# Kernel tuning notes

Hardware: AMD Instinct MI355X
Metric: run time of the kernel (lower is better)

The kernel has to match this reference:

```python
import jax, jax.numpy as jnp
import numpy as np
import math

FEAT_DIM, M, K = 512, 64, 256
D = FEAT_DIM // M  # 8
ALPHA = 1.0
B = 16384


def setup_inputs() -> dict:
    key = jax.random.key(0)
    kx, kc = jax.random.split(key)
    x = jax.random.normal(kx, (B, FEAT_DIM), dtype=jnp.float32)
    # Codebook: unit-norm codewords scaled by 1/sqrt(M), mimicking the
    # normalized-hypersphere init (orthogonal rotation / permutation do not
    # change the math, only the values).
    c = jax.random.normal(kc, (M, K, D), dtype=jnp.float32)
    c = c / jnp.linalg.norm(c, axis=-1, keepdims=True) / math.sqrt(M)
    return {"x": x, "C": c}


def reference(x, C):
    # x: (B, feat_dim) -> (B, M, D)
    x_ = x.reshape(x.shape[0], M, D)
    # per-subspace inner products with codewords: (B, M, K)
    ips = jnp.einsum('bmd,mkd->bmk', x_, C)
    # training-mode straight-through assignment
    soft = jax.nn.softmax(ips * (M / ALPHA), axis=-1)
    hard = jax.nn.one_hot(jnp.argmax(ips, axis=-1), K, dtype=ips.dtype)
    codes = jax.lax.stop_gradient(hard - soft) + soft
    # reconstruction: (B, M, D) -> (B, feat_dim)
    x_hat = jnp.einsum('mkd,bmk->bmd', C, codes).reshape(x.shape[0], -1)
    return x_hat, codes
```

## Files before the change

### kernel.cpp

```cpp
#include <hip/hip_runtime.h>
#include <math.h>


#define B_SZ   16384
#define FEAT   512
#define M_SZ   64
#define K_SZ   256
#define D_SZ   8

typedef float v4f __attribute__((ext_vector_type(4)));

__global__ __launch_bounds__(256) void pq_argmax(
    const float* __restrict__ x,
    const float* __restrict__ C,
    unsigned char* __restrict__ bestk8)
{
#pragma clang fp contract(off)

    const int m     = blockIdx.x & (M_SZ - 1);
    const int chunk = blockIdx.x >> 6;
    const int b     = (chunk << 8) | threadIdx.x;

    const float* xp = x + (size_t)b * FEAT + m * D_SZ;
    const v4f xa = ((const v4f*)xp)[0];
    const v4f xb = ((const v4f*)xp)[1];

    const float* __restrict__ Cm = C + (size_t)m * (K_SZ * D_SZ);

    float best  = -INFINITY;
    int   bestk = 0;

#pragma unroll 8
    for (int k = 0; k < K_SZ; ++k) {
        const v4f* cr = (const v4f*)(Cm + k * D_SZ);
        const v4f ca = cr[0];
        const v4f cb = cr[1];
        v4f P = xa * ca;
        v4f Q = xb * cb;
        v4f T = P + Q;
        float dot = (T.x + T.y) + (T.z + T.w);
        if (dot > best) { best = dot; bestk = k; }
    }

    bestk8[(size_t)b * M_SZ + m] = (unsigned char)bestk;
}

__global__ __launch_bounds__(256) void pq_fill(
    const float* __restrict__ C,
    const unsigned char* __restrict__ bestk8,
    float* __restrict__ xhat,
    float* __restrict__ codes)
{
    const int t    = threadIdx.x;
    const int b0   = blockIdx.x << 2;
    const int w    = t >> 6;
    const int lane = t & 63;

    __shared__ unsigned char lbk[4 * M_SZ];

    lbk[t] = bestk8[(size_t)b0 * M_SZ + t];

    {
        const int b  = b0 + w;
        const int kb = (int)bestk8[(size_t)b * M_SZ + lane];
        const float* cw = C + ((size_t)lane * K_SZ + kb) * D_SZ;
        const float4 h0 = ((const float4*)cw)[0];
        const float4 h1 = ((const float4*)cw)[1];
        float* xh = xhat + (size_t)b * FEAT + lane * D_SZ;
        ((float4*)xh)[0] = h0;
        ((float4*)xh)[1] = h1;
    }

    __syncthreads();

    const int lane4 = lane << 2;
    float4* const slab = (float4*)(codes + (size_t)b0 * (M_SZ * K_SZ));

#pragma unroll 4
    for (int j = 0; j < 64; ++j) {
        const int r  = j >> 4;
        const int mj = (w + 4 * j) & 63;
        const int kk = (int)lbk[(r << 6) | mj];
        float4 v;
        v.x = (kk == lane4 + 0) ? 1.0f : 0.0f;
        v.y = (kk == lane4 + 1) ? 1.0f : 0.0f;
        v.z = (kk == lane4 + 2) ? 1.0f : 0.0f;
        v.w = (kk == lane4 + 3) ? 1.0f : 0.0f;
        slab[t + 256 * j] = v;
    }
}

extern "C" void kernel_launch(void* const* d_in, const int* in_sizes, int n_in,
                              void* d_out, int out_size, void* d_ws, size_t ws_size,
                              hipStream_t stream)
{
    const float* x = (const float*)d_in[0];
    const float* C = (const float*)d_in[1];
    float* xhat  = (float*)d_out;
    float* codes = (float*)d_out + (size_t)B_SZ * FEAT;
    unsigned char* bestk8 = (unsigned char*)d_ws;

    hipLaunchKernelGGL(pq_argmax, dim3(4096), dim3(256), 0, stream, x, C, bestk8);
    hipLaunchKernelGGL(pq_fill,   dim3(4096), dim3(256), 0, stream, C, bestk8, xhat, codes);
}
```

Before: 1.203 ms.

## Fuse argmax and one-hot fill into a single kernel using shared indices

Merges the argmax kernel and the fill kernel into one launch. Each 512-thread block computes best-codeword indices for 64 rows into shared memory, then writes x_hat and the one-hot codes slab from there. This removes the global workspace round-trip and the second launch. The grid shrinks to 256 large blocks, which lowers occupancy and serialises the compute and store phases within each block.

```diff
diff --git a/kernel.cpp b/kernel.cpp
--- a/kernel.cpp
+++ b/kernel.cpp
@@ -10,83 +10,76 @@
 
 typedef float v4f __attribute__((ext_vector_type(4)));
 
-__global__ __launch_bounds__(256) void pq_argmax(
+__global__ __launch_bounds__(512) void pq_fused(
     const float* __restrict__ x,
     const float* __restrict__ C,
-    unsigned char* __restrict__ bestk8)
+    float* __restrict__ xhat,
+    float* __restrict__ codes)
 {
 #pragma clang fp contract(off)
 
-    const int m     = blockIdx.x & (M_SZ - 1);
-    const int chunk = blockIdx.x >> 6;
-    const int b     = (chunk << 8) | threadIdx.x;
+    const int t    = threadIdx.x;
+    const int w    = t >> 6;
+    const int lane = t & 63;
+    const int b0   = blockIdx.x << 6;
+    const int b    = b0 + lane;
 
-    const float* xp = x + (size_t)b * FEAT + m * D_SZ;
-    const v4f xa = ((const v4f*)xp)[0];
-    const v4f xb = ((const v4f*)xp)[1];
+    __shared__ unsigned char lbk[M_SZ * 64];
 
-    const float* __restrict__ Cm = C + (size_t)m * (K_SZ * D_SZ);
+    {
+        const float* xrow = x + (size_t)b * FEAT;
+#pragma unroll
+        for (int j = 0; j < 8; ++j) {
+            const int m = (w << 3) | j;
+            const v4f* xp = (const v4f*)(xrow + m * D_SZ);
+            const v4f xa = xp[0];
+            const v4f xb = xp[1];
+            const float* __restrict__ Cm = C + (size_t)m * (K_SZ * D_SZ);
 
-    float best  = -INFINITY;
-    int   bestk = 0;
-
+            float best  = -INFINITY;
+            int   bestk = 0;
 #pragma unroll 8
-    for (int k = 0; k < K_SZ; ++k) {
-        const v4f* cr = (const v4f*)(Cm + k * D_SZ);
-        const v4f ca = cr[0];
-        const v4f cb = cr[1];
-        v4f P = xa * ca;
-        v4f Q = xb * cb;
-        v4f T = P + Q;
-        float dot = (T.x + T.y) + (T.z + T.w);
-        if (dot > best) { best = dot; bestk = k; }
+            for (int k = 0; k < K_SZ; ++k) {
+                const v4f* cr = (const v4f*)(Cm + k * D_SZ);
+                v4f P = xa * cr[0];
+                v4f Q = xb * cr[1];
+                v4f T = P + Q;
+                float dot = (T.x + T.y) + (T.z + T.w);
+                if (dot > best) { best = dot; bestk = k; }
+            }
+            lbk[(m << 6) | lane] = (unsigned char)bestk;
+        }
     }
 
-    bestk8[(size_t)b * M_SZ + m] = (unsigned char)bestk;
-}
+    __syncthreads();
 
-__global__ __launch_bounds__(256) void pq_fill(
-    const float* __restrict__ C,
-    const unsigned char* __restrict__ bestk8,
-    float* __restrict__ xhat,
-    float* __restrict__ codes)
-{
-    const int t    = threadIdx.x;
-    const int b0   = blockIdx.x << 2;
-    const int w    = t >> 6;
-    const int lane = t & 63;
-
-    __shared__ unsigned char lbk[4 * M_SZ];
-
-    lbk[t] = bestk8[(size_t)b0 * M_SZ + t];
-
-    {
-        const int b  = b0 + w;
-        const int kb = (int)bestk8[(size_t)b * M_SZ + lane];
+#pragma unroll
+    for (int jj = 0; jj < 8; ++jj) {
+        const int bl = w + (jj << 3);
+        const int kb = (int)lbk[(lane << 6) | bl];
         const float* cw = C + ((size_t)lane * K_SZ + kb) * D_SZ;
         const float4 h0 = ((const float4*)cw)[0];
         const float4 h1 = ((const float4*)cw)[1];
-        float* xh = xhat + (size_t)b * FEAT + lane * D_SZ;
+        float* xh = xhat + (size_t)(b0 + bl) * FEAT + lane * D_SZ;
         ((float4*)xh)[0] = h0;
         ((float4*)xh)[1] = h1;
     }
-
-    __syncthreads();
 
     const int lane4 = lane << 2;
     float4* const slab = (float4*)(codes + (size_t)b0 * (M_SZ * K_SZ));
 
 #pragma unroll 4
-    for (int j = 0; j < 64; ++j) {
-        const int r  = j >> 4;
-        const int mj = (w + 4 * j) & 63;
-        const int kk = (int)lbk[(r << 6) | mj];
+    for (int j = 0; j < 512; ++j) {
+        const int g   = w + (j << 3);
+        const int mj  = g & 63;
+        const int row = g >> 6;
+        const int kk  = (int)lbk[(mj << 6) | row];
         float4 v;
         v.x = (kk == lane4 + 0) ? 1.0f : 0.0f;
         v.y = (kk == lane4 + 1) ? 1.0f : 0.0f;
         v.z = (kk == lane4 + 2) ? 1.0f : 0.0f;
         v.w = (kk == lane4 + 3) ? 1.0f : 0.0f;
-        slab[t + 256 * j] = v;
+        slab[t + (j << 9)] = v;
     }
 }
 
@@ -98,8 +91,6 @@
     const float* C = (const float*)d_in[1];
     float* xhat  = (float*)d_out;
     float* codes = (float*)d_out + (size_t)B_SZ * FEAT;
-    unsigned char* bestk8 = (unsigned char*)d_ws;
 
-    hipLaunchKernelGGL(pq_argmax, dim3(4096), dim3(256), 0, stream, x, C, bestk8);
-    hipLaunchKernelGGL(pq_fill,   dim3(4096), dim3(256), 0, stream, C, bestk8, xhat, codes);
+    hipLaunchKernelGGL(pq_fused, dim3(256), dim3(512), 0, stream, x, C, xhat, codes);
 }
```

Measured after the change: 1.319 ms. 1.1x slower.
